# Optimization experiments

Hardware: AMD Instinct MI355X
Metric: run time of the kernel (lower is better)

The kernel has to match this reference:

```python
import jax, jax.numpy as jnp
import numpy as np

N = 50000   # nodes
E = 800000  # edges
D = 128     # hidden_dim
O = 128     # out_dim (must equal hidden_dim; see prior_mean Linear)
T = 16      # number of timesteps for the modeled time encoding
EPS = 1e-9


def _gcn(x, W, b, src, dst, ew, n):
    """PyG-style GCNConv: add self-loops, symmetric deg^-1/2 normalization."""
    loop = jnp.arange(n)
    s = jnp.concatenate([src, loop])
    d = jnp.concatenate([dst, loop])
    w = jnp.concatenate([ew, jnp.ones((n,), x.dtype)])
    deg = jax.ops.segment_sum(w, d, num_segments=n)
    dinv = jnp.where(deg > 0, jax.lax.rsqrt(deg), 0.0)
    norm = dinv[s] * w * dinv[d]              # [E+N]
    h = x @ W                                  # [N, out]
    out = jax.ops.segment_sum(h[s] * norm[:, None], d, num_segments=n)
    return out + b


def setup_inputs() -> dict:
    key = jax.random.key(0)
    ks = jax.random.split(key, 20)

    def lin(k, fan_in, fan_out):
        return jax.random.normal(k, (fan_in, fan_out), jnp.float32) / np.sqrt(fan_in)

    return {
        "edge_index": jax.random.randint(ks[0], (2, E), 0, N, dtype=jnp.int64),
        "x": jax.random.normal(ks[1], (N, D), jnp.float32),
        "t": 3,
        "edge_score": jax.random.uniform(ks[2], (E,), jnp.float32),
        "total_len": 16,
        "train_len": 12,
        "W_enc": lin(ks[3], D, D), "b_enc": jnp.zeros((D,), jnp.float32),
        "W_mu": lin(ks[4], D, O), "b_mu": jnp.zeros((O,), jnp.float32),
        "W_std": lin(ks[5], D, O), "b_std": jnp.zeros((O,), jnp.float32),
        "W_prior": lin(ks[6], D, O), "b_prior": jnp.zeros((O,), jnp.float32),
        "W_pm": lin(ks[7], D, O), "b_pm": jnp.zeros((O,), jnp.float32),
        "W_ps": lin(ks[8], D, O), "b_ps": jnp.zeros((O,), jnp.float32),
        "time_emb": 0.02 * jax.random.normal(ks[9], (T, O), jnp.float32),
    }


def reference(edge_index, x, t, edge_score, total_len, train_len,
              W_enc, b_enc, W_mu, b_mu, W_std, b_std,
              W_prior, b_prior, W_pm, b_pm, W_ps, b_ps, time_emb):
    src, dst = edge_index[0], edge_index[1]
    n = x.shape[0]
    ones_e = jnp.ones((src.shape[0],), x.dtype)

    # encoder
    enc_t = jax.nn.relu(_gcn(x, W_enc, b_enc, src, dst, edge_score, n))
    # drop = 0.0 -> dropout is identity
    enc_mean_t = _gcn(enc_t, W_mu, b_mu, src, dst, ones_e, n)
    enc_std_t = jax.nn.sigmoid(_gcn(enc_t, W_std, b_std, src, dst, ones_e, n))

    # reparameterize (fixed eps for determinism)
    eps = jax.random.normal(jax.random.key(42), enc_mean_t.shape, enc_mean_t.dtype)
    conf_z_t = eps * enc_std_t + enc_mean_t

    # prior branch: time_encoding(prior, t) modeled as additive time embedding
    prior = jax.nn.relu(_gcn(x, W_prior, b_prior, src, dst, ones_e, n))
    prior = prior + time_emb[t]
    prior_mean = prior @ W_pm + b_pm
    prior_std = jax.nn.sigmoid(prior @ W_ps + b_ps)

    # fused KL divergence
    kl = (2.0 * jnp.log(prior_std + EPS) - 2.0 * jnp.log(enc_std_t + EPS)
          + ((enc_std_t + EPS) ** 2 + (enc_mean_t - prior_mean) ** 2)
          / (prior_std + EPS) ** 2 - 1.0)
    kl_loss = 0.5 * jnp.mean(jnp.sum(kl, axis=1), axis=0)
    return kl_loss, conf_z_t
```

## Files before the change

### kernel.cpp

```cpp
#include <hip/hip_runtime.h>
#include <math.h>

#define D 128

typedef unsigned int u32;
typedef unsigned short u16;
typedef __attribute__((ext_vector_type(8))) short bf16x8;
typedef __attribute__((ext_vector_type(4))) float f32x4;
typedef __attribute__((ext_vector_type(4))) u32 u32x4;

__device__ __forceinline__ u32 rotl32(u32 x, int r){ return (x<<r) | (x>>(32-r)); }

__device__ __forceinline__ u16 f2bf(float x){
  u32 u = __float_as_uint(x);
  return (u16)((u + 0x7fffu + ((u >> 16) & 1u)) >> 16);
}
__device__ __forceinline__ float bf2f(u16 h){ return __uint_as_float(((u32)h) << 16); }

__device__ __forceinline__ float jax_normal_part_xor(u32 m){
  const u32 ks0 = 0u, ks1 = 42u, ks2 = 0x1BD11BF0u;
  u32 x0 = 0u + ks0;
  u32 x1 = m  + ks1;
  #define TF_R4(a,b,c,d) \
    x0 += x1; x1 = rotl32(x1,(a)); x1 ^= x0; \
    x0 += x1; x1 = rotl32(x1,(b)); x1 ^= x0; \
    x0 += x1; x1 = rotl32(x1,(c)); x1 ^= x0; \
    x0 += x1; x1 = rotl32(x1,(d)); x1 ^= x0;
  TF_R4(13,15,26,6)   x0 += ks1; x1 += ks2 + 1u;
  TF_R4(17,29,16,24)  x0 += ks2; x1 += ks0 + 2u;
  TF_R4(13,15,26,6)   x0 += ks0; x1 += ks1 + 3u;
  TF_R4(17,29,16,24)  x0 += ks1; x1 += ks2 + 4u;
  TF_R4(13,15,26,6)   x0 += ks2; x1 += ks0 + 5u;
  #undef TF_R4
  u32 bits = x0 ^ x1;
  float f = __uint_as_float((bits >> 9) | 0x3F800000u) - 1.0f;
  const float LO = -0.99999994f;
  float u = fmaxf(LO, f * 2.0f + LO);
  float w = -__logf(fmaf(-u, u, 1.0f));
  float p;
  if (w < 5.0f){
    w -= 2.5f;
    p =  2.81022636e-08f;
    p = fmaf(p, w,  3.43273939e-07f);
    p = fmaf(p, w, -3.5233877e-06f);
    p = fmaf(p, w, -4.39150654e-06f);
    p = fmaf(p, w,  0.00021858087f);
    p = fmaf(p, w, -0.00125372503f);
    p = fmaf(p, w, -0.00417768164f);
    p = fmaf(p, w,  0.246640727f);
    p = fmaf(p, w,  1.50140941f);
  } else {
    w = sqrtf(w) - 3.0f;
    p = -0.000200214257f;
    p = fmaf(p, w,  0.000100950558f);
    p = fmaf(p, w,  0.00134934322f);
    p = fmaf(p, w, -0.00367342844f);
    p = fmaf(p, w,  0.00573950773f);
    p = fmaf(p, w, -0.0076224613f);
    p = fmaf(p, w,  0.00943887047f);
    p = fmaf(p, w,  1.00167406f);
    p = fmaf(p, w,  2.83297682f);
  }
  return 1.41421354f * (p * u);
}

__device__ __forceinline__ float sigmoidf_(float z){ return 1.0f / (1.0f + __expf(-z)); }

__global__ __launch_bounds__(256) void k_eps(u32* __restrict__ epsb, int half_total){
  int idx = blockIdx.x*256 + threadIdx.x;
  int stride = gridDim.x*256;
  for (int i = idx; i < half_total; i += stride){
    u32 m0 = 2u*(u32)i;
    float e0 = jax_normal_part_xor(m0);
    float e1 = jax_normal_part_xor(m0 + 1u);
    epsb[i] = (u32)f2bf(e0) | ((u32)f2bf(e1) << 16);
  }
}

__global__ void k_detect(const u32* __restrict__ e_u32, int* __restrict__ flag){
  __shared__ int s_nz;
  if (threadIdx.x == 0) s_nz = 0;
  __syncthreads();
  if (e_u32[2*threadIdx.x + 1] != 0u) atomicAdd(&s_nz, 1);
  __syncthreads();
  if (threadIdx.x == 0) *flag = (s_nz == 0) ? 1 : 0;
}

__global__ void k_norm(const void* __restrict__ eidx, const int* __restrict__ flag,
                       int* __restrict__ src_w, int* __restrict__ dst_w, int e){
  int i = blockIdx.x*256 + threadIdx.x;
  if (i >= e) return;
  if (*flag){
    const u32* u = (const u32*)eidx;
    src_w[i] = (int)u[2*(size_t)i];
    dst_w[i] = (int)u[2*((size_t)e + i)];
  } else {
    const int* p = (const int*)eidx;
    src_w[i] = p[i];
    dst_w[i] = p[e + i];
  }
}

__global__ void k_init(int* __restrict__ cnt, int n){
  int i = blockIdx.x*256 + threadIdx.x;
  if (i < n) cnt[i] = 0;
}

__global__ void k_hist(const int* __restrict__ dst, int* __restrict__ cnt, int e){
  int i = blockIdx.x*256 + threadIdx.x;
  if (i >= e) return;
  atomicAdd(&cnt[dst[i]], 1);
}

__global__ __launch_bounds__(256) void k_scan1(const int* __restrict__ cnt,
                                               int* __restrict__ rp,
                                               int* __restrict__ bsum, int n){
  __shared__ int sh[256];
  int tid = threadIdx.x, idx = blockIdx.x*256 + tid;
  int v = (idx < n) ? cnt[idx] : 0;
  sh[tid] = v; __syncthreads();
  for (int off = 1; off < 256; off <<= 1){
    int t = (tid >= off) ? sh[tid-off] : 0;
    __syncthreads(); sh[tid] += t; __syncthreads();
  }
  if (idx < n) rp[idx] = sh[tid] - v;
  if (tid == 255) bsum[blockIdx.x] = sh[255];
}

__global__ __launch_bounds__(1024) void k_scan2(int* __restrict__ bsum, int nb){
  __shared__ int sh[1024];
  int tid = threadIdx.x;
  int v = (tid < nb) ? bsum[tid] : 0;
  sh[tid] = v; __syncthreads();
  for (int off = 1; off < 1024; off <<= 1){
    int t = (tid >= off) ? sh[tid-off] : 0;
    __syncthreads(); sh[tid] += t; __syncthreads();
  }
  if (tid < nb) bsum[tid] = sh[tid] - v;
}

__global__ void k_scan3(int* __restrict__ rp, int* __restrict__ cur,
                        const int* __restrict__ bsum, const int* __restrict__ cnt,
                        float* __restrict__ dinv_o, int n, int e){
  int idx = blockIdx.x*256 + threadIdx.x;
  if (idx < n){
    int r = rp[idx] + bsum[blockIdx.x];
    rp[idx] = r; cur[idx] = r;
    dinv_o[idx] = rsqrtf((float)(cnt[idx] + 1));
  }
  if (idx == 0) rp[n] = e;
}

__global__ void k_scatter(const int* __restrict__ src, const int* __restrict__ dst,
                          const float* __restrict__ sc, int* __restrict__ cur,
                          int* __restrict__ col, float* __restrict__ wsrt, int e){
  int i = blockIdx.x*256 + threadIdx.x;
  if (i >= e) return;
  int d = dst[i];
  int p = atomicAdd(&cur[d], 1);
  col[p] = src[i];
  wsrt[p] = sc[i];
}

__global__ void k_deg(const int* __restrict__ rp, const float* __restrict__ wsrt,
                      float* __restrict__ dinv_s, int n){
  int i = blockIdx.x*256 + threadIdx.x;
  if (i >= n) return;
  float s = 1.0f;
  int e0 = rp[i], e1 = rp[i+1];
  for (int j = e0; j < e1; ++j) s += wsrt[j];
  dinv_s[i] = rsqrtf(s);
}

__global__ void k_wconv(const float* __restrict__ W0, const float* __restrict__ W1,
                        const float* __restrict__ W2, const float* __restrict__ W3,
                        const float* __restrict__ W4, const float* __restrict__ W5,
                        u16* __restrict__ wt){
  const float* Ws[6] = {W0,W1,W2,W3,W4,W5};
  const float* W = Ws[blockIdx.y];
  u16* Wt = wt + (size_t)blockIdx.y*16384;
  int idx = blockIdx.x*256 + threadIdx.x;
  int k = idx >> 7, col = idx & 127;
  Wt[col*128 + k] = f2bf(W[idx]);
}

__global__ __launch_bounds__(256) void k_agg_dual(
    const float* __restrict__ x, const int* __restrict__ rp,
    const int* __restrict__ col, const float* __restrict__ wsrt,
    const float* __restrict__ dinv_s, const float* __restrict__ dinv_o,
    u16* __restrict__ out_s, u16* __restrict__ out_o, int n){
  int wid = (blockIdx.x * 256 + threadIdx.x) >> 6;
  int lane = threadIdx.x & 63;
  if (wid >= n) return;
  const float2* x2 = (const float2*)x;
  float dsv = dinv_s[wid], dov = dinv_o[wid];
  float2 xv = x2[(size_t)wid*64 + lane];
  float ss = dsv*dsv, oo = dov*dov;
  float2 as = { xv.x*ss, xv.y*ss };
  float2 ao = { xv.x*oo, xv.y*oo };
  int e0 = rp[wid], e1 = rp[wid+1];
  for (int base = e0; base < e1; base += 64){
    int cnt = e1 - base; if (cnt > 64) cnt = 64;
    int idx = base + (lane < cnt ? lane : cnt - 1);
    int   sl = col[idx];
    float wl = wsrt[idx];
    float nsl = dinv_s[sl] * wl * dsv;
    float nol = dinv_o[sl] * dov;
    int j = 0;
    for (; j + 4 <= cnt; j += 4){
      int   s0=__shfl(sl,j),   s1=__shfl(sl,j+1),   s2=__shfl(sl,j+2),   s3=__shfl(sl,j+3);
      float a0=__shfl(nsl,j),  a1=__shfl(nsl,j+1),  a2=__shfl(nsl,j+2),  a3=__shfl(nsl,j+3);
      float b0=__shfl(nol,j),  b1=__shfl(nol,j+1),  b2=__shfl(nol,j+2),  b3=__shfl(nol,j+3);
      float2 r0 = x2[(size_t)s0*64 + lane];
      float2 r1 = x2[(size_t)s1*64 + lane];
      float2 r2 = x2[(size_t)s2*64 + lane];
      float2 r3 = x2[(size_t)s3*64 + lane];
      as.x = fmaf(a0,r0.x,as.x); as.y = fmaf(a0,r0.y,as.y);
      ao.x = fmaf(b0,r0.x,ao.x); ao.y = fmaf(b0,r0.y,ao.y);
      as.x = fmaf(a1,r1.x,as.x); as.y = fmaf(a1,r1.y,as.y);
      ao.x = fmaf(b1,r1.x,ao.x); ao.y = fmaf(b1,r1.y,ao.y);
      as.x = fmaf(a2,r2.x,as.x); as.y = fmaf(a2,r2.y,as.y);
      ao.x = fmaf(b2,r2.x,ao.x); ao.y = fmaf(b2,r2.y,ao.y);
      as.x = fmaf(a3,r3.x,as.x); as.y = fmaf(a3,r3.y,as.y);
      ao.x = fmaf(b3,r3.x,ao.x); ao.y = fmaf(b3,r3.y,ao.y);
    }
    for (; j < cnt; ++j){
      int   s0=__shfl(sl,j);
      float a0=__shfl(nsl,j), b0=__shfl(nol,j);
      float2 r0 = x2[(size_t)s0*64 + lane];
      as.x = fmaf(a0,r0.x,as.x); as.y = fmaf(a0,r0.y,as.y);
      ao.x = fmaf(b0,r0.x,ao.x); ao.y = fmaf(b0,r0.y,ao.y);
    }
  }
  ((u32*)out_s)[(size_t)wid*64 + lane] = (u32)f2bf(as.x) | ((u32)f2bf(as.y) << 16);
  ((u32*)out_o)[(size_t)wid*64 + lane] = (u32)f2bf(ao.x) | ((u32)f2bf(ao.y) << 16);
}

__global__ __launch_bounds__(256) void k_agg_one(
    const u16* __restrict__ h, const int* __restrict__ rp,
    const int* __restrict__ col, const float* __restrict__ dinv_o,
    u16* __restrict__ out, int n){
  int wid = (blockIdx.x * 256 + threadIdx.x) >> 6;
  int lane = threadIdx.x & 63;
  if (wid >= n) return;
  const u32* h2 = (const u32*)h;
  float dov = dinv_o[wid];
  u32 hv = h2[(size_t)wid*64 + lane];
  float oo = dov*dov;
  float2 ao = { bf2f((u16)(hv & 0xffff))*oo, bf2f((u16)(hv >> 16))*oo };
  int e0 = rp[wid], e1 = rp[wid+1];
  for (int base = e0; base < e1; base += 64){
    int cnt = e1 - base; if (cnt > 64) cnt = 64;
    int idx = base + (lane < cnt ? lane : cnt - 1);
    int   sl = col[idx];
    float nol = dinv_o[sl] * dov;
    int j = 0;
    for (; j + 4 <= cnt; j += 4){
      int   s0=__shfl(sl,j),  s1=__shfl(sl,j+1),  s2=__shfl(sl,j+2),  s3=__shfl(sl,j+3);
      float b0=__shfl(nol,j), b1=__shfl(nol,j+1), b2=__shfl(nol,j+2), b3=__shfl(nol,j+3);
      u32 r0 = h2[(size_t)s0*64 + lane];
      u32 r1 = h2[(size_t)s1*64 + lane];
      u32 r2 = h2[(size_t)s2*64 + lane];
      u32 r3 = h2[(size_t)s3*64 + lane];
      ao.x = fmaf(b0, bf2f((u16)(r0&0xffff)), ao.x); ao.y = fmaf(b0, bf2f((u16)(r0>>16)), ao.y);
      ao.x = fmaf(b1, bf2f((u16)(r1&0xffff)), ao.x); ao.y = fmaf(b1, bf2f((u16)(r1>>16)), ao.y);
      ao.x = fmaf(b2, bf2f((u16)(r2&0xffff)), ao.x); ao.y = fmaf(b2, bf2f((u16)(r2>>16)), ao.y);
      ao.x = fmaf(b3, bf2f((u16)(r3&0xffff)), ao.x); ao.y = fmaf(b3, bf2f((u16)(r3>>16)), ao.y);
    }
    for (; j < cnt; ++j){
      int   s0=__shfl(sl,j);
      float b0=__shfl(nol,j);
      u32 r0 = h2[(size_t)s0*64 + lane];
      ao.x = fmaf(b0, bf2f((u16)(r0&0xffff)), ao.x); ao.y = fmaf(b0, bf2f((u16)(r0>>16)), ao.y);
    }
  }
  ((u32*)out)[(size_t)wid*64 + lane] = (u32)f2bf(ao.x) | ((u32)f2bf(ao.y) << 16);
}


__global__ __launch_bounds__(256) void k_mfma_act2(
    const u16* __restrict__ A0, const u16* __restrict__ Wt0, const float* __restrict__ b0,
    const u16* __restrict__ A1, const u16* __restrict__ Wt1, const float* __restrict__ b1,
    const float* __restrict__ temb, const int* __restrict__ t_ptr,
    u16* __restrict__ out0, u16* __restrict__ out1, int n){
  const int sl = blockIdx.y;
  const u16* A  = sl ? A1 : A0;
  const u16* Wt = sl ? Wt1 : Wt0;
  const float* b = sl ? b1 : b0;
  u16* out = sl ? out1 : out0;
  const int tid = threadIdx.x;
  const int lane = tid & 63, wave = tid >> 6;
  const int lr = lane & 15, lg = lane >> 4;
  const int rw = wave >> 1, cw = wave & 1;
  const int row0 = blockIdx.x*32 + rw*16;
  int rowf = row0 + lr;
  int rowc = rowf < n ? rowf : n - 1;
  const char* Arow = (const char*)A + (size_t)rowc*256;
  const char* Wb   = (const char*)Wt + (cw*64 + lr)*256 + lg*16;
  f32x4 z = {0.f,0.f,0.f,0.f};
  f32x4 acc[4];
  #pragma unroll
  for (int i = 0; i < 4; ++i) acc[i] = z;
  #pragma unroll
  for (int ks = 0; ks < 4; ++ks){
    bf16x8 a = *(const bf16x8*)(Arow + ks*64 + lg*16);
    #pragma unroll
    for (int cf = 0; cf < 4; ++cf){
      bf16x8 bb = *(const bf16x8*)(Wb + cf*16*256 + ks*64);
      acc[cf] = __builtin_amdgcn_mfma_f32_16x16x32_bf16(a, bb, acc[cf], 0, 0, 0);
    }
  }
  int t = sl ? *t_ptr : 0;
  int rbase = row0 + (lg << 2);
  #pragma unroll
  for (int cf = 0; cf < 4; ++cf){
    int colw = cw*64 + cf*16 + lr;
    float bb = b[colw];
    float tt = sl ? temb[t*128 + colw] : 0.f;
    #pragma unroll
    for (int r = 0; r < 4; ++r){
      int row = rbase + r;
      if (row < n)
        out[(size_t)row*128 + colw] = f2bf(fmaxf(acc[cf][r] + bb, 0.f) + tt);
    }
  }
}

__global__ __launch_bounds__(256) void k_mfma_quad(
    const u16* __restrict__ Apr, const u16* __restrict__ Aen,
    const u16* __restrict__ Wtpm, const float* __restrict__ bpm,
    const u16* __restrict__ Wtps, const float* __restrict__ bps,
    const u16* __restrict__ Wtmu, const float* __restrict__ bmu,
    const u16* __restrict__ Wtsd, const float* __restrict__ bsd,
    const u32* __restrict__ epsb,
    float* __restrict__ conf, float* __restrict__ pblk, int n){
  const int tid = threadIdx.x;
  const int lane = tid & 63, wave = tid >> 6;
  const int lr = lane & 15, lg = lane >> 4;
  const int rw = wave >> 1, cw = wave & 1;
  const int row0 = blockIdx.x*32 + rw*16;
  int rowf = row0 + lr;
  int rowc = rowf < n ? rowf : n - 1;
  const char* Ap = (const char*)Apr + (size_t)rowc*256;
  const char* Ae = (const char*)Aen + (size_t)rowc*256;
  const int wcb = (cw*64 + lr)*256 + lg*16;
  const char* Wpm = (const char*)Wtpm + wcb;
  const char* Wps = (const char*)Wtps + wcb;
  const char* Wmu = (const char*)Wtmu + wcb;
  const char* Wsd = (const char*)Wtsd + wcb;
  f32x4 z = {0.f,0.f,0.f,0.f};
  f32x4 aPM[4], aPS[4], aMU[4], aSD[4];
  #pragma unroll
  for (int i = 0; i < 4; ++i){ aPM[i]=z; aPS[i]=z; aMU[i]=z; aSD[i]=z; }
  #pragma unroll
  for (int ks = 0; ks < 4; ++ks){
    bf16x8 a5 = *(const bf16x8*)(Ap + ks*64 + lg*16);
    bf16x8 a2 = *(const bf16x8*)(Ae + ks*64 + lg*16);
    #pragma unroll
    for (int cf = 0; cf < 4; ++cf){
      int off = cf*16*256 + ks*64;
      aPM[cf] = __builtin_amdgcn_mfma_f32_16x16x32_bf16(a5, *(const bf16x8*)(Wpm+off), aPM[cf], 0,0,0);
      aPS[cf] = __builtin_amdgcn_mfma_f32_16x16x32_bf16(a5, *(const bf16x8*)(Wps+off), aPS[cf], 0,0,0);
      aMU[cf] = __builtin_amdgcn_mfma_f32_16x16x32_bf16(a2, *(const bf16x8*)(Wmu+off), aMU[cf], 0,0,0);
      aSD[cf] = __builtin_amdgcn_mfma_f32_16x16x32_bf16(a2, *(const bf16x8*)(Wsd+off), aSD[cf], 0,0,0);
    }
  }
  const float EPS = 1e-9f;
  int rbase = row0 + (lg << 2);
  float klsum = 0.f;
  #pragma unroll
  for (int cf = 0; cf < 4; ++cf){
    int colw = cw*64 + cf*16 + lr;
    float bb1 = bpm[colw], bb2 = bps[colw];
    float bb3 = bmu[colw], bb4 = bsd[colw];
    #pragma unroll
    for (int r = 0; r < 4; ++r){
      int row = rbase + r;
      if (row < n){
        size_t m = (size_t)row*128 + colw;
        float pmv = aPM[cf][r] + bb1;
        float psv = sigmoidf_(aPS[cf][r] + bb2);
        float em  = aMU[cf][r] + bb3;
        float es  = sigmoidf_(aSD[cf][r] + bb4);
        u32 ew = epsb[m >> 1];
        float eps = bf2f((u16)((colw & 1) ? (ew >> 16) : (ew & 0xffff)));
        conf[m] = fmaf(eps, es, em);
        float es_e = es + EPS, ps_e = psv + EPS;
        float diff = em - pmv;
        klsum += 2.0f*__logf(ps_e/es_e)
               + (es_e*es_e + diff*diff) / (ps_e*ps_e) - 1.0f;
      }
    }
  }
  #pragma unroll
  for (int off = 32; off > 0; off >>= 1) klsum += __shfl_down(klsum, off);
  __shared__ float wsum[4];
  if ((tid & 63) == 0) wsum[tid >> 6] = klsum;
  __syncthreads();
  if (tid == 0) pblk[blockIdx.x] = wsum[0] + wsum[1] + wsum[2] + wsum[3];
}

__global__ __launch_bounds__(256) void k_finish(const float* __restrict__ pblk, int nb,
                                                float* __restrict__ out0, int n){
  __shared__ double sh[256];
  double s = 0.0;
  for (int i = threadIdx.x; i < nb; i += 256) s += (double)pblk[i];
  sh[threadIdx.x] = s; __syncthreads();
  for (int off = 128; off > 0; off >>= 1){
    if (threadIdx.x < off) sh[threadIdx.x] += sh[threadIdx.x + off];
    __syncthreads();
  }
  if (threadIdx.x == 0) out0[0] = (float)(0.5 * sh[0] / (double)n);
}

extern "C" void kernel_launch(void* const* d_in, const int* in_sizes, int n_in,
                              void* d_out, int out_size, void* d_ws, size_t ws_size,
                              hipStream_t stream){
  const void*  eidx   = d_in[0];
  const float* x      = (const float*)d_in[1];
  const int*   t_ptr  = (const int*)d_in[2];
  const float* escore = (const float*)d_in[3];
  const float* W_enc = (const float*)d_in[6];  const float* b_enc = (const float*)d_in[7];
  const float* W_mu  = (const float*)d_in[8];  const float* b_mu  = (const float*)d_in[9];
  const float* W_std = (const float*)d_in[10]; const float* b_std = (const float*)d_in[11];
  const float* W_pr  = (const float*)d_in[12]; const float* b_pr  = (const float*)d_in[13];
  const float* W_pm  = (const float*)d_in[14]; const float* b_pm  = (const float*)d_in[15];
  const float* W_ps  = (const float*)d_in[16]; const float* b_ps  = (const float*)d_in[17];
  const float* temb  = (const float*)d_in[18];

  const int N = in_sizes[1] / D;
  const int E = in_sizes[3];

  char* w = (char*)d_ws;
  auto alloc = [&](size_t bytes) -> char* {
    char* p = w; w += (bytes + 255) & ~(size_t)255; return p;
  };
  int*    flag   = (int*)   alloc(256);
  int*    src_w  = (int*)   alloc((size_t)E*4);
  int*    dst_w  = (int*)   alloc((size_t)E*4);
  int*    cnt    = (int*)   alloc((size_t)N*4);
  int*    rp     = (int*)   alloc((size_t)(N+1)*4);
  int*    cur    = (int*)   alloc((size_t)N*4);
  float*  dinv_s = (float*) alloc((size_t)N*4);
  float*  dinv_o = (float*) alloc((size_t)N*4);
  int*    bsum   = (int*)   alloc(1024*4);
  int*    col    = (int*)   alloc((size_t)E*4);
  float*  wsrt   = (float*) alloc((size_t)E*4);
  u16*    wt     = (u16*)   alloc((size_t)6*16384*2);
  u16*    B1     = (u16*)   alloc((size_t)N*D*2);
  u16*    B2     = (u16*)   alloc((size_t)N*D*2);
  u16*    B3     = (u16*)   alloc((size_t)N*D*2);
  u16*    B5     = (u16*)   alloc((size_t)N*D*2);
  u32*    EPSB   = (u32*)   alloc((size_t)N*64*4);
  const int gG32 = (N + 31) / 32;
  float*  pblk   = (float*) alloc((size_t)gG32*4);
  (void)ws_size; (void)n_in; (void)out_size;

  float* conf = ((float*)d_out) + 1;

  u16* Wt_enc = wt + 0*16384;
  u16* Wt_pr  = wt + 1*16384;
  u16* Wt_pm  = wt + 2*16384;
  u16* Wt_ps  = wt + 3*16384;
  u16* Wt_mu  = wt + 4*16384;
  u16* Wt_std = wt + 5*16384;

  const int gE  = (E + 255) / 256;
  const int gN  = (N + 255) / 256;
  const int gW  = (N * 64 + 255) / 256;

  k_eps    <<<2048, 256, 0, stream>>>(EPSB, N*64);
  k_wconv  <<<dim3(64,6), 256, 0, stream>>>(W_enc, W_pr, W_pm, W_ps, W_mu, W_std, wt);
  k_detect <<<1, 256, 0, stream>>>((const u32*)eidx, flag);
  k_norm   <<<gE, 256, 0, stream>>>(eidx, flag, src_w, dst_w, E);
  k_init   <<<gN, 256, 0, stream>>>(cnt, N);
  k_hist   <<<gE, 256, 0, stream>>>(dst_w, cnt, E);
  k_scan1  <<<gN, 256, 0, stream>>>(cnt, rp, bsum, N);
  k_scan2  <<<1, 1024, 0, stream>>>(bsum, gN);
  k_scan3  <<<gN, 256, 0, stream>>>(rp, cur, bsum, cnt, dinv_o, N, E);
  k_scatter<<<gE, 256, 0, stream>>>(src_w, dst_w, escore, cur, col, wsrt, E);
  k_deg    <<<gN, 256, 0, stream>>>(rp, wsrt, dinv_s, N);

  k_agg_dual<<<gW, 256, 0, stream>>>(x, rp, col, wsrt, dinv_s, dinv_o, B1, B2, N);
  k_mfma_act2<<<dim3(gG32,2), 256, 0, stream>>>(B1, Wt_enc, b_enc, B2, Wt_pr, b_pr,
                                                temb, t_ptr, B3, B5, N);
  k_agg_one<<<gW, 256, 0, stream>>>(B3, rp, col, dinv_o, B2, N);
  k_mfma_quad<<<gG32, 256, 0, stream>>>(B5, B2, Wt_pm, b_pm, Wt_ps, b_ps,
                                        Wt_mu, b_mu, Wt_std, b_std, EPSB,
                                        conf, pblk, N);
  k_finish<<<1, 256, 0, stream>>>(pblk, gG32, (float*)d_out, N);
}
```

Before: 337.7 us.

## Gather bf16 features, fuse histogram into edge decode, retile MFMA kernels to 16 rows

Converts x to bf16 once, so the first dual aggregation gathers half as many bytes per neighbour row. Folds the degree histogram atomics into the edge-index decode kernel, which removes one pass over the edge list. Retiles both MFMA kernels so each block covers 16 rows, with each wave owning 32 columns, giving twice as many blocks. The eps values are now loaded before the matmul loop so their latency overlaps it. In exchange there is an extra conversion pass over x and lower input precision in the first aggregation.

```diff
diff --git a/kernel.cpp b/kernel.cpp
--- a/kernel.cpp
+++ b/kernel.cpp
@@ -7,7 +7,6 @@
 typedef unsigned short u16;
 typedef __attribute__((ext_vector_type(8))) short bf16x8;
 typedef __attribute__((ext_vector_type(4))) float f32x4;
-typedef __attribute__((ext_vector_type(4))) u32 u32x4;
 
 __device__ __forceinline__ u32 rotl32(u32 x, int r){ return (x<<r) | (x>>(32-r)); }
 
@@ -77,6 +76,14 @@
   }
 }
 
+__global__ __launch_bounds__(256) void k_xconv(const float* __restrict__ x,
+                                               u32* __restrict__ xb, int total2){
+  int i = blockIdx.x*256 + threadIdx.x;
+  if (i >= total2) return;
+  float2 v = ((const float2*)x)[i];
+  xb[i] = (u32)f2bf(v.x) | ((u32)f2bf(v.y) << 16);
+}
+
 __global__ void k_detect(const u32* __restrict__ e_u32, int* __restrict__ flag){
   __shared__ int s_nz;
   if (threadIdx.x == 0) s_nz = 0;
@@ -86,30 +93,29 @@
   if (threadIdx.x == 0) *flag = (s_nz == 0) ? 1 : 0;
 }
 
-__global__ void k_norm(const void* __restrict__ eidx, const int* __restrict__ flag,
-                       int* __restrict__ src_w, int* __restrict__ dst_w, int e){
-  int i = blockIdx.x*256 + threadIdx.x;
-  if (i >= e) return;
-  if (*flag){
-    const u32* u = (const u32*)eidx;
-    src_w[i] = (int)u[2*(size_t)i];
-    dst_w[i] = (int)u[2*((size_t)e + i)];
-  } else {
-    const int* p = (const int*)eidx;
-    src_w[i] = p[i];
-    dst_w[i] = p[e + i];
-  }
-}
-
 __global__ void k_init(int* __restrict__ cnt, int n){
   int i = blockIdx.x*256 + threadIdx.x;
   if (i < n) cnt[i] = 0;
 }
 
-__global__ void k_hist(const int* __restrict__ dst, int* __restrict__ cnt, int e){
+__global__ void k_norm(const void* __restrict__ eidx, const int* __restrict__ flag,
+                       int* __restrict__ src_w, int* __restrict__ dst_w,
+                       int* __restrict__ cnt, int e){
   int i = blockIdx.x*256 + threadIdx.x;
   if (i >= e) return;
-  atomicAdd(&cnt[dst[i]], 1);
+  int s, d;
+  if (*flag){
+    const u32* u = (const u32*)eidx;
+    s = (int)u[2*(size_t)i];
+    d = (int)u[2*((size_t)e + i)];
+  } else {
+    const int* p = (const int*)eidx;
+    s = p[i];
+    d = p[e + i];
+  }
+  src_w[i] = s;
+  dst_w[i] = d;
+  atomicAdd(&cnt[d], 1);
 }
 
 __global__ __launch_bounds__(256) void k_scan1(const int* __restrict__ cnt,
@@ -185,19 +191,19 @@
 }
 
 __global__ __launch_bounds__(256) void k_agg_dual(
-    const float* __restrict__ x, const int* __restrict__ rp,
+    const u32* __restrict__ xb, const int* __restrict__ rp,
     const int* __restrict__ col, const float* __restrict__ wsrt,
     const float* __restrict__ dinv_s, const float* __restrict__ dinv_o,
     u16* __restrict__ out_s, u16* __restrict__ out_o, int n){
   int wid = (blockIdx.x * 256 + threadIdx.x) >> 6;
   int lane = threadIdx.x & 63;
   if (wid >= n) return;
-  const float2* x2 = (const float2*)x;
   float dsv = dinv_s[wid], dov = dinv_o[wid];
-  float2 xv = x2[(size_t)wid*64 + lane];
+  u32 xv = xb[(size_t)wid*64 + lane];
+  float xlo = bf2f((u16)(xv & 0xffff)), xhi = bf2f((u16)(xv >> 16));
   float ss = dsv*dsv, oo = dov*dov;
-  float2 as = { xv.x*ss, xv.y*ss };
-  float2 ao = { xv.x*oo, xv.y*oo };
+  float2 as = { xlo*ss, xhi*ss };
+  float2 ao = { xlo*oo, xhi*oo };
   int e0 = rp[wid], e1 = rp[wid+1];
   for (int base = e0; base < e1; base += 64){
     int cnt = e1 - base; if (cnt > 64) cnt = 64;
@@ -211,25 +217,30 @@
       int   s0=__shfl(sl,j),   s1=__shfl(sl,j+1),   s2=__shfl(sl,j+2),   s3=__shfl(sl,j+3);
       float a0=__shfl(nsl,j),  a1=__shfl(nsl,j+1),  a2=__shfl(nsl,j+2),  a3=__shfl(nsl,j+3);
       float b0=__shfl(nol,j),  b1=__shfl(nol,j+1),  b2=__shfl(nol,j+2),  b3=__shfl(nol,j+3);
-      float2 r0 = x2[(size_t)s0*64 + lane];
-      float2 r1 = x2[(size_t)s1*64 + lane];
-      float2 r2 = x2[(size_t)s2*64 + lane];
-      float2 r3 = x2[(size_t)s3*64 + lane];
-      as.x = fmaf(a0,r0.x,as.x); as.y = fmaf(a0,r0.y,as.y);
-      ao.x = fmaf(b0,r0.x,ao.x); ao.y = fmaf(b0,r0.y,ao.y);
-      as.x = fmaf(a1,r1.x,as.x); as.y = fmaf(a1,r1.y,as.y);
-      ao.x = fmaf(b1,r1.x,ao.x); ao.y = fmaf(b1,r1.y,ao.y);
-      as.x = fmaf(a2,r2.x,as.x); as.y = fmaf(a2,r2.y,as.y);
-      ao.x = fmaf(b2,r2.x,ao.x); ao.y = fmaf(b2,r2.y,ao.y);
-      as.x = fmaf(a3,r3.x,as.x); as.y = fmaf(a3,r3.y,as.y);
-      ao.x = fmaf(b3,r3.x,ao.x); ao.y = fmaf(b3,r3.y,ao.y);
+      u32 r0 = xb[(size_t)s0*64 + lane];
+      u32 r1 = xb[(size_t)s1*64 + lane];
+      u32 r2 = xb[(size_t)s2*64 + lane];
+      u32 r3 = xb[(size_t)s3*64 + lane];
+      float l0 = bf2f((u16)(r0&0xffff)), h0 = bf2f((u16)(r0>>16));
+      float l1 = bf2f((u16)(r1&0xffff)), h1 = bf2f((u16)(r1>>16));
+      float l2 = bf2f((u16)(r2&0xffff)), h2 = bf2f((u16)(r2>>16));
+      float l3 = bf2f((u16)(r3&0xffff)), h3 = bf2f((u16)(r3>>16));
+      as.x = fmaf(a0,l0,as.x); as.y = fmaf(a0,h0,as.y);
+      ao.x = fmaf(b0,l0,ao.x); ao.y = fmaf(b0,h0,ao.y);
+      as.x = fmaf(a1,l1,as.x); as.y = fmaf(a1,h1,as.y);
+      ao.x = fmaf(b1,l1,ao.x); ao.y = fmaf(b1,h1,ao.y);
+      as.x = fmaf(a2,l2,as.x); as.y = fmaf(a2,h2,as.y);
+      ao.x = fmaf(b2,l2,ao.x); ao.y = fmaf(b2,h2,ao.y);
+      as.x = fmaf(a3,l3,as.x); as.y = fmaf(a3,h3,as.y);
+      ao.x = fmaf(b3,l3,ao.x); ao.y = fmaf(b3,h3,ao.y);
     }
     for (; j < cnt; ++j){
       int   s0=__shfl(sl,j);
       float a0=__shfl(nsl,j), b0=__shfl(nol,j);
-      float2 r0 = x2[(size_t)s0*64 + lane];
-      as.x = fmaf(a0,r0.x,as.x); as.y = fmaf(a0,r0.y,as.y);
-      ao.x = fmaf(b0,r0.x,ao.x); ao.y = fmaf(b0,r0.y,ao.y);
+      u32 r0 = xb[(size_t)s0*64 + lane];
+      float l0 = bf2f((u16)(r0&0xffff)), h0 = bf2f((u16)(r0>>16));
+      as.x = fmaf(a0,l0,as.x); as.y = fmaf(a0,h0,as.y);
+      ao.x = fmaf(b0,l0,ao.x); ao.y = fmaf(b0,h0,ao.y);
     }
   }
   ((u32*)out_s)[(size_t)wid*64 + lane] = (u32)f2bf(as.x) | ((u32)f2bf(as.y) << 16);
@@ -291,21 +302,19 @@
   const int tid = threadIdx.x;
   const int lane = tid & 63, wave = tid >> 6;
   const int lr = lane & 15, lg = lane >> 4;
-  const int rw = wave >> 1, cw = wave & 1;
-  const int row0 = blockIdx.x*32 + rw*16;
+  const int row0 = blockIdx.x * 16;
   int rowf = row0 + lr;
   int rowc = rowf < n ? rowf : n - 1;
   const char* Arow = (const char*)A + (size_t)rowc*256;
-  const char* Wb   = (const char*)Wt + (cw*64 + lr)*256 + lg*16;
+  const char* Wb   = (const char*)Wt + (wave*32 + lr)*256 + lg*16;
   f32x4 z = {0.f,0.f,0.f,0.f};
-  f32x4 acc[4];
-  #pragma unroll
-  for (int i = 0; i < 4; ++i) acc[i] = z;
+  f32x4 acc[2];
+  acc[0] = z; acc[1] = z;
   #pragma unroll
   for (int ks = 0; ks < 4; ++ks){
     bf16x8 a = *(const bf16x8*)(Arow + ks*64 + lg*16);
     #pragma unroll
-    for (int cf = 0; cf < 4; ++cf){
+    for (int cf = 0; cf < 2; ++cf){
       bf16x8 bb = *(const bf16x8*)(Wb + cf*16*256 + ks*64);
       acc[cf] = __builtin_amdgcn_mfma_f32_16x16x32_bf16(a, bb, acc[cf], 0, 0, 0);
     }
@@ -313,8 +322,8 @@
   int t = sl ? *t_ptr : 0;
   int rbase = row0 + (lg << 2);
   #pragma unroll
-  for (int cf = 0; cf < 4; ++cf){
-    int colw = cw*64 + cf*16 + lr;
+  for (int cf = 0; cf < 2; ++cf){
+    int colw = wave*32 + cf*16 + lr;
     float bb = b[colw];
     float tt = sl ? temb[t*128 + colw] : 0.f;
     #pragma unroll
@@ -337,27 +346,37 @@
   const int tid = threadIdx.x;
   const int lane = tid & 63, wave = tid >> 6;
   const int lr = lane & 15, lg = lane >> 4;
-  const int rw = wave >> 1, cw = wave & 1;
-  const int row0 = blockIdx.x*32 + rw*16;
+  const int row0 = blockIdx.x * 16;
   int rowf = row0 + lr;
   int rowc = rowf < n ? rowf : n - 1;
   const char* Ap = (const char*)Apr + (size_t)rowc*256;
   const char* Ae = (const char*)Aen + (size_t)rowc*256;
-  const int wcb = (cw*64 + lr)*256 + lg*16;
+  const int wcb = (wave*32 + lr)*256 + lg*16;
   const char* Wpm = (const char*)Wtpm + wcb;
   const char* Wps = (const char*)Wtps + wcb;
   const char* Wmu = (const char*)Wtmu + wcb;
   const char* Wsd = (const char*)Wtsd + wcb;
+  int rbase = row0 + (lg << 2);
+  u32 ew[2][4];
+  #pragma unroll
+  for (int cf = 0; cf < 2; ++cf){
+    int colw = wave*32 + cf*16 + lr;
+    #pragma unroll
+    for (int r = 0; r < 4; ++r){
+      int row = rbase + r; if (row >= n) row = n - 1;
+      ew[cf][r] = epsb[(size_t)row*64 + (colw >> 1)];
+    }
+  }
   f32x4 z = {0.f,0.f,0.f,0.f};
-  f32x4 aPM[4], aPS[4], aMU[4], aSD[4];
-  #pragma unroll
-  for (int i = 0; i < 4; ++i){ aPM[i]=z; aPS[i]=z; aMU[i]=z; aSD[i]=z; }
+  f32x4 aPM[2], aPS[2], aMU[2], aSD[2];
+  #pragma unroll
+  for (int i = 0; i < 2; ++i){ aPM[i]=z; aPS[i]=z; aMU[i]=z; aSD[i]=z; }
   #pragma unroll
   for (int ks = 0; ks < 4; ++ks){
     bf16x8 a5 = *(const bf16x8*)(Ap + ks*64 + lg*16);
     bf16x8 a2 = *(const bf16x8*)(Ae + ks*64 + lg*16);
     #pragma unroll
-    for (int cf = 0; cf < 4; ++cf){
+    for (int cf = 0; cf < 2; ++cf){
       int off = cf*16*256 + ks*64;
       aPM[cf] = __builtin_amdgcn_mfma_f32_16x16x32_bf16(a5, *(const bf16x8*)(Wpm+off), aPM[cf], 0,0,0);
       aPS[cf] = __builtin_amdgcn_mfma_f32_16x16x32_bf16(a5, *(const bf16x8*)(Wps+off), aPS[cf], 0,0,0);
@@ -366,11 +385,10 @@
     }
   }
   const float EPS = 1e-9f;
-  int rbase = row0 + (lg << 2);
   float klsum = 0.f;
   #pragma unroll
-  for (int cf = 0; cf < 4; ++cf){
-    int colw = cw*64 + cf*16 + lr;
+  for (int cf = 0; cf < 2; ++cf){
+    int colw = wave*32 + cf*16 + lr;
     float bb1 = bpm[colw], bb2 = bps[colw];
     float bb3 = bmu[colw], bb4 = bsd[colw];
     #pragma unroll
@@ -382,8 +400,7 @@
         float psv = sigmoidf_(aPS[cf][r] + bb2);
         float em  = aMU[cf][r] + bb3;
         float es  = sigmoidf_(aSD[cf][r] + bb4);
-        u32 ew = epsb[m >> 1];
-        float eps = bf2f((u16)((colw & 1) ? (ew >> 16) : (ew & 0xffff)));
+        float eps = bf2f((u16)((colw & 1) ? (ew[cf][r] >> 16) : (ew[cf][r] & 0xffff)));
         conf[m] = fmaf(eps, es, em);
         float es_e = es + EPS, ps_e = psv + EPS;
         float diff = em - pmv;
@@ -447,13 +464,14 @@
   int*    col    = (int*)   alloc((size_t)E*4);
   float*  wsrt   = (float*) alloc((size_t)E*4);
   u16*    wt     = (u16*)   alloc((size_t)6*16384*2);
+  u32*    XB     = (u32*)   alloc((size_t)N*64*4);
   u16*    B1     = (u16*)   alloc((size_t)N*D*2);
   u16*    B2     = (u16*)   alloc((size_t)N*D*2);
   u16*    B3     = (u16*)   alloc((size_t)N*D*2);
   u16*    B5     = (u16*)   alloc((size_t)N*D*2);
   u32*    EPSB   = (u32*)   alloc((size_t)N*64*4);
-  const int gG32 = (N + 31) / 32;
-  float*  pblk   = (float*) alloc((size_t)gG32*4);
+  const int gG16 = (N + 15) / 16;
+  float*  pblk   = (float*) alloc((size_t)gG16*4);
   (void)ws_size; (void)n_in; (void)out_size;
 
   float* conf = ((float*)d_out) + 1;
@@ -470,23 +488,23 @@
   const int gW  = (N * 64 + 255) / 256;
 
   k_eps    <<<2048, 256, 0, stream>>>(EPSB, N*64);
+  k_xconv  <<<gW, 256, 0, stream>>>(x, XB, N*64);
   k_wconv  <<<dim3(64,6), 256, 0, stream>>>(W_enc, W_pr, W_pm, W_ps, W_mu, W_std, wt);
   k_detect <<<1, 256, 0, stream>>>((const u32*)eidx, flag);
-  k_norm   <<<gE, 256, 0, stream>>>(eidx, flag, src_w, dst_w, E);
   k_init   <<<gN, 256, 0, stream>>>(cnt, N);
-  k_hist   <<<gE, 256, 0, stream>>>(dst_w, cnt, E);
+  k_norm   <<<gE, 256, 0, stream>>>(eidx, flag, src_w, dst_w, cnt, E);
   k_scan1  <<<gN, 256, 0, stream>>>(cnt, rp, bsum, N);
   k_scan2  <<<1, 1024, 0, stream>>>(bsum, gN);
   k_scan3  <<<gN, 256, 0, stream>>>(rp, cur, bsum, cnt, dinv_o, N, E);
   k_scatter<<<gE, 256, 0, stream>>>(src_w, dst_w, escore, cur, col, wsrt, E);
   k_deg    <<<gN, 256, 0, stream>>>(rp, wsrt, dinv_s, N);
 
-  k_agg_dual<<<gW, 256, 0, stream>>>(x, rp, col, wsrt, dinv_s, dinv_o, B1, B2, N);
-  k_mfma_act2<<<dim3(gG32,2), 256, 0, stream>>>(B1, Wt_enc, b_enc, B2, Wt_pr, b_pr,
+  k_agg_dual<<<gW, 256, 0, stream>>>(XB, rp, col, wsrt, dinv_s, dinv_o, B1, B2, N);
+  k_mfma_act2<<<dim3(gG16,2), 256, 0, stream>>>(B1, Wt_enc, b_enc, B2, Wt_pr, b_pr,
                                                 temb, t_ptr, B3, B5, N);
   k_agg_one<<<gW, 256, 0, stream>>>(B3, rp, col, dinv_o, B2, N);
-  k_mfma_quad<<<gG32, 256, 0, stream>>>(B5, B2, Wt_pm, b_pm, Wt_ps, b_ps,
+  k_mfma_quad<<<gG16, 256, 0, stream>>>(B5, B2, Wt_pm, b_pm, Wt_ps, b_ps,
                                         Wt_mu, b_mu, Wt_std, b_std, EPSB,
                                         conf, pblk, N);
-  k_finish<<<1, 256, 0, stream>>>(pblk, gG32, (float*)d_out, N);
-}
+  k_finish<<<1, 256, 0, stream>>>(pblk, gG16, (float*)d_out, N);
+}
```

New measurement: 326.3 us. -3.4%, faster.
